# Performance work log

Measured on AMD Instinct MI355X. Metric: run time of the kernel, lower is better.

Reference implementation:

```python
import jax, jax.numpy as jnp
import numpy as np

NA, NH, E, EL, D = 100000, 20000, 1000000, 200000, 128


def _sage(x_src, x_dst, src, dst, W_l, b_l, W_r, num_dst):
    # PyG SAGEConv: out = lin_l(mean_j x_src[j]) + lin_r(x_dst); lin_l has bias, lin_r does not.
    msg = x_src[src]                                   # [E, D] gather
    agg = jax.ops.segment_sum(msg, dst, num_segments=num_dst)   # [num_dst, D]
    deg = jax.ops.segment_sum(jnp.ones((src.shape[0],), x_src.dtype), dst, num_segments=num_dst)
    agg = agg / jnp.maximum(deg, 1.0)[:, None]         # mean aggregation; isolated nodes -> 0
    return agg @ W_l + b_l + x_dst @ W_r


def setup_inputs() -> dict:
    key = jax.random.key(0)
    ks = jax.random.split(key, 24)
    s = 1.0 / np.sqrt(D)
    inp = {
        "x_author": jax.random.normal(ks[0], (NA, D), jnp.float32),
        "x_hotel": jax.random.normal(ks[1], (NH, D), jnp.float32),
        "ei_ah_src": jax.random.randint(ks[2], (E,), 0, NA, jnp.int32),
        "ei_ah_dst": jax.random.randint(ks[3], (E,), 0, NH, jnp.int32),
        "ei_ha_src": jax.random.randint(ks[4], (E,), 0, NH, jnp.int32),
        "ei_ha_dst": jax.random.randint(ks[5], (E,), 0, NA, jnp.int32),
        "eli_row": jax.random.randint(ks[6], (EL,), 0, NA, jnp.int32),
        "eli_col": jax.random.randint(ks[7], (EL,), 0, NH, jnp.int32),
    }
    # per-layer, per-edge-type SAGE weights
    names = ["W1_ah_l", "W1_ah_r", "W1_ha_l", "W1_ha_r", "W2_ah_l", "W2_ah_r", "W2_ha_l", "W2_ha_r"]
    for i, n in enumerate(names):
        inp[n] = jax.random.normal(ks[8 + i], (D, D), jnp.float32) * s
    inp["b1_ah_l"] = jnp.zeros((D,), jnp.float32)
    inp["b1_ha_l"] = jnp.zeros((D,), jnp.float32)
    inp["b2_ah_l"] = jnp.zeros((D,), jnp.float32)
    inp["b2_ha_l"] = jnp.zeros((D,), jnp.float32)
    # decoder MLP
    inp["W_lin1"] = jax.random.normal(ks[16], (2 * D, D), jnp.float32) * (1.0 / np.sqrt(2 * D))
    inp["b_lin1"] = jnp.zeros((D,), jnp.float32)
    inp["W_lin2"] = jax.random.normal(ks[17], (D, 1), jnp.float32) * s
    inp["b_lin2"] = jnp.zeros((1,), jnp.float32)
    return inp


def reference(x_author, x_hotel, ei_ah_src, ei_ah_dst, ei_ha_src, ei_ha_dst,
              eli_row, eli_col,
              W1_ah_l, b1_ah_l, W1_ah_r, W1_ha_l, b1_ha_l, W1_ha_r,
              W2_ah_l, b2_ah_l, W2_ah_r, W2_ha_l, b2_ha_l, W2_ha_r,
              W_lin1, b_lin1, W_lin2, b_lin2):
    # layer 1 (HeteroConv: each node type receives from exactly one edge type) + relu
    h_hotel = jax.nn.relu(_sage(x_author, x_hotel, ei_ah_src, ei_ah_dst, W1_ah_l, b1_ah_l, W1_ah_r, NH))
    h_author = jax.nn.relu(_sage(x_hotel, x_author, ei_ha_src, ei_ha_dst, W1_ha_l, b1_ha_l, W1_ha_r, NA))
    # layer 2 (no relu on last layer)
    z_hotel = _sage(h_author, h_hotel, ei_ah_src, ei_ah_dst, W2_ah_l, b2_ah_l, W2_ah_r, NH)
    z_author = _sage(h_hotel, h_author, ei_ha_src, ei_ha_dst, W2_ha_l, b2_ha_l, W2_ha_r, NA)
    # edge decoder: gather-concat -> 2-layer MLP
    z1 = jnp.concatenate([z_author[eli_row], z_hotel[eli_col]], axis=-1)  # [EL, 2D]
    z2 = jax.nn.relu(z1 @ W_lin1 + b_lin1)                                # [EL, D]
    pred = (z2 @ W_lin2 + b_lin2).reshape(-1)                             # [EL]
    return (pred, z1, z2)
```

## Files before the change

### kernel.cpp

```cpp
#include <hip/hip_runtime.h>

#define NA_ 100000
#define NH_ 20000
#define E_  1000000
#define EL_ 200000
#define D_  128

#define NBH_ 20
#define NBA_ 98
#define NBT_ 118

typedef __attribute__((ext_vector_type(8))) short short8;
typedef __attribute__((ext_vector_type(4))) float f32x4;

__device__ __forceinline__ ushort f2bf(float f) {
  union { float f; uint u; } v; v.f = f;
  uint u = v.u;
  return (ushort)((u + 0x7FFFu + ((u >> 16) & 1u)) >> 16);
}
__device__ __forceinline__ uint pack2bf(float a, float b) {
  return (uint)f2bf(a) | ((uint)f2bf(b) << 16);
}


__global__ __launch_bounds__(256) void cvt_count_k(const float* __restrict__ xa, ushort* __restrict__ da,
                                                   const float* __restrict__ xh, ushort* __restrict__ dh,
                                                   const int* __restrict__ d1, int* __restrict__ c1,
                                                   const int* __restrict__ d2, int* __restrict__ c2) {
  int i = blockIdx.x * 256 + threadIdx.x;
  if (i < E_) atomicAdd(&c1[d1[i]], 1);
  else if (i < 2 * E_) atomicAdd(&c2[d2[i - E_]], 1);
  const int na4 = NA_ * 32;
  if (i < na4) {
    float4 v = *(const float4*)(xa + (size_t)i * 4);
    ((uint2*)da)[i] = make_uint2(pack2bf(v.x, v.y), pack2bf(v.z, v.w));
  } else {
    int k = i - na4;
    if (k < NH_ * 32) {
      float4 v = *(const float4*)(xh + (size_t)k * 4);
      ((uint2*)dh)[k] = make_uint2(pack2bf(v.x, v.y), pack2bf(v.z, v.w));
    }
  }
}


__global__ __launch_bounds__(256) void csr_partial_k(const int* __restrict__ cnt_h,
                                                     const int* __restrict__ cnt_a,
                                                     int* __restrict__ partials) {
  int b = blockIdx.x;
  bool isH = b < NBH_;
  const int* c = isH ? cnt_h : cnt_a;
  int n = isH ? NH_ : NA_;
  int chunk = isH ? b : b - NBH_;
  int t = threadIdx.x;
  int i0 = chunk * 1024 + t * 4;
  int s = 0;
  if (i0 + 3 < n) {
    int4 v = *(const int4*)(c + i0);
    s = v.x + v.y + v.z + v.w;
  } else {
    for (int k = 0; k < 4; k++) if (i0 + k < n) s += c[i0 + k];
  }
#pragma unroll
  for (int d = 1; d < 64; d <<= 1) s += __shfl_xor(s, d);
  __shared__ int ws[4];
  int lane = t & 63, wv = t >> 6;
  if (lane == 0) ws[wv] = s;
  __syncthreads();
  if (t == 0) partials[b] = ws[0] + ws[1] + ws[2] + ws[3];
}


__global__ __launch_bounds__(128) void csr_scanp_k(int* __restrict__ partials,
                                                   int* __restrict__ off_h,
                                                   int* __restrict__ off_a) {
  __shared__ int s[128];
  int t = threadIdx.x;
  int orig = (t < NBT_) ? partials[t] : 0;
  int seg = (t < NBH_) ? 0 : 1;
  s[t] = orig;
  __syncthreads();
  for (int d = 1; d < 128; d <<= 1) {
    int v = 0;
    if (t >= d) {
      int o = t - d;
      if (((o < NBH_) ? 0 : 1) == seg) v = s[o];
    }
    __syncthreads();
    s[t] += v;
    __syncthreads();
  }
  if (t < NBT_) partials[t] = s[t] - orig;
  if (t == 0) { off_h[NH_] = E_; off_a[NA_] = E_; }
}


__global__ __launch_bounds__(256) void csr_scatter_k(int* __restrict__ cnt_h, int* __restrict__ off_h,
                                                     int* __restrict__ cnt_a, int* __restrict__ off_a,
                                                     const int* __restrict__ partials) {
  int b = blockIdx.x;
  bool isH = b < NBH_;
  int* c = isH ? cnt_h : cnt_a;
  int* off = isH ? off_h : off_a;
  int n = isH ? NH_ : NA_;
  int chunk = isH ? b : b - NBH_;
  int t = threadIdx.x, lane = t & 63, wv = t >> 6;
  int base = partials[b];
  int i0 = chunk * 1024 + t * 4;
  int v0 = 0, v1 = 0, v2 = 0, v3 = 0;
  if (i0 + 3 < n) {
    int4 v = *(const int4*)(c + i0);
    v0 = v.x; v1 = v.y; v2 = v.z; v3 = v.w;
  } else {
    if (i0 < n) v0 = c[i0];
    if (i0 + 1 < n) v1 = c[i0 + 1];
    if (i0 + 2 < n) v2 = c[i0 + 2];
    if (i0 + 3 < n) v3 = c[i0 + 3];
  }
  int tsum = v0 + v1 + v2 + v3;
  int x = tsum;
#pragma unroll
  for (int d = 1; d < 64; d <<= 1) { int y = __shfl_up(x, d); if (lane >= d) x += y; }
  __shared__ int ws[4], wb[4];
  if (lane == 63) ws[wv] = x;
  __syncthreads();
  if (t == 0) { int r = 0; for (int i = 0; i < 4; i++) { wb[i] = r; r += ws[i]; } }
  __syncthreads();
  int run = base + wb[wv] + (x - tsum);
  int o0 = run, o1 = o0 + v0, o2 = o1 + v1, o3 = o2 + v2;
  if (i0 + 3 < n) {
    *(int4*)(off + i0) = make_int4(o0, o1, o2, o3);
    *(int4*)(c + i0) = make_int4(o0, o1, o2, o3);
  } else {
    if (i0 < n) { off[i0] = o0; c[i0] = o0; }
    if (i0 + 1 < n) { off[i0 + 1] = o1; c[i0 + 1] = o1; }
    if (i0 + 2 < n) { off[i0 + 2] = o2; c[i0 + 2] = o2; }
    if (i0 + 3 < n) { off[i0 + 3] = o3; c[i0 + 3] = o3; }
  }
}

__global__ void fill_edges_k(const int* __restrict__ s1, const int* __restrict__ d1,
                             int* __restrict__ cur1, int* __restrict__ out1,
                             const int* __restrict__ s2, const int* __restrict__ d2,
                             int* __restrict__ cur2, int* __restrict__ out2) {
  int i = blockIdx.x * 256 + threadIdx.x;
  if (i < E_) {
    int p = atomicAdd(&cur1[d1[i]], 1);
    out1[p] = s1[i];
  } else if (i < 2 * E_) {
    int ii = i - E_;
    int p = atomicAdd(&cur2[d2[ii]], 1);
    out2[p] = s2[ii];
  }
}


__global__ void pack_all_k(const float* a0, const float* a1, ushort* ad,
                           const float* b0, const float* b1, ushort* bd,
                           const float* c0, const float* c1, ushort* cd,
                           const float* d0, const float* d1, ushort* dd,
                           const float* e0, const float* e1, ushort* ed) {
  const float *s0, *s1; ushort* dst;
  switch (blockIdx.y) {
    case 0: s0 = a0; s1 = a1; dst = ad; break;
    case 1: s0 = b0; s1 = b1; dst = bd; break;
    case 2: s0 = c0; s1 = c1; dst = cd; break;
    case 3: s0 = d0; s1 = d1; dst = dd; break;
    default: s0 = e0; s1 = e1; dst = ed; break;
  }
  int idx = blockIdx.x * 256 + threadIdx.x;
  int j = idx & 7, lane = (idx >> 3) & 63, nt = (idx >> 9) & 7, kc = idx >> 12;
  int k = kc * 32 + (lane >> 4) * 8 + j;
  int n = nt * 16 + (lane & 15);
  float v = (k < 128) ? s0[k * 128 + n] : s1[(k - 128) * 128 + n];
  dst[idx] = f2bf(v);
}


__global__ __launch_bounds__(256) void aggregate_bf_k(const ushort* __restrict__ xsrc,
                                                      const int* __restrict__ off,
                                                      const int* __restrict__ srcs,
                                                      ushort* __restrict__ out, int ndst) {
  int w = (blockIdx.x * 256 + threadIdx.x) >> 6;
  int lane = threadIdx.x & 63;
  if (w >= ndst) return;
  const int grp = lane >> 4, sub = lane & 15;
  int beg = off[w], end = off[w + 1];
  float a[8] = {0.f, 0.f, 0.f, 0.f, 0.f, 0.f, 0.f, 0.f};
  const ushort* base = xsrc + sub * 8;
  int j = beg + grp;
  for (; j + 4 < end; j += 8) {
    int sA = srcs[j];
    int sB = srcs[j + 4];
    uint4 vA = *(const uint4*)(base + (size_t)sA * 128);
    uint4 vB = *(const uint4*)(base + (size_t)sB * 128);
    a[0] += __uint_as_float(vA.x << 16); a[1] += __uint_as_float(vA.x & 0xFFFF0000u);
    a[2] += __uint_as_float(vA.y << 16); a[3] += __uint_as_float(vA.y & 0xFFFF0000u);
    a[4] += __uint_as_float(vA.z << 16); a[5] += __uint_as_float(vA.z & 0xFFFF0000u);
    a[6] += __uint_as_float(vA.w << 16); a[7] += __uint_as_float(vA.w & 0xFFFF0000u);
    a[0] += __uint_as_float(vB.x << 16); a[1] += __uint_as_float(vB.x & 0xFFFF0000u);
    a[2] += __uint_as_float(vB.y << 16); a[3] += __uint_as_float(vB.y & 0xFFFF0000u);
    a[4] += __uint_as_float(vB.z << 16); a[5] += __uint_as_float(vB.z & 0xFFFF0000u);
    a[6] += __uint_as_float(vB.w << 16); a[7] += __uint_as_float(vB.w & 0xFFFF0000u);
  }
  if (j < end) {
    int sA = srcs[j];
    uint4 vA = *(const uint4*)(base + (size_t)sA * 128);
    a[0] += __uint_as_float(vA.x << 16); a[1] += __uint_as_float(vA.x & 0xFFFF0000u);
    a[2] += __uint_as_float(vA.y << 16); a[3] += __uint_as_float(vA.y & 0xFFFF0000u);
    a[4] += __uint_as_float(vA.z << 16); a[5] += __uint_as_float(vA.z & 0xFFFF0000u);
    a[6] += __uint_as_float(vA.w << 16); a[7] += __uint_as_float(vA.w & 0xFFFF0000u);
  }
#pragma unroll
  for (int k = 0; k < 8; k++) {
    a[k] += __shfl_xor(a[k], 16);
    a[k] += __shfl_xor(a[k], 32);
  }
  int deg = end - beg;
  float sc = 1.0f / (float)(deg > 0 ? deg : 1);
  if (grp == 0) {
    uint4 o;
    o.x = pack2bf(a[0] * sc, a[1] * sc);
    o.y = pack2bf(a[2] * sc, a[3] * sc);
    o.z = pack2bf(a[4] * sc, a[5] * sc);
    o.w = pack2bf(a[6] * sc, a[7] * sc);
    *(uint4*)(out + (size_t)w * 128 + sub * 8) = o;
  }
}


template <bool RELU, bool OUTBF>
__global__ __launch_bounds__(256) void sage_mfma_k(const ushort* __restrict__ Abf,
                                                   const ushort* __restrict__ Xbf,
                                                   const ushort* __restrict__ Wp,
                                                   const float* __restrict__ bias,
                                                   float* __restrict__ outF,
                                                   ushort* __restrict__ outB, int rows) {
  const int t = threadIdx.x;
  const int w = t >> 6, lane = t & 63, quad = lane >> 4, m = lane & 15;
  const int row0 = blockIdx.x * 64 + w * 16;
  int rA = row0 + m; if (rA >= rows) rA = rows - 1;
  f32x4 acc[8];
#pragma unroll
  for (int nt = 0; nt < 8; nt++) acc[nt] = (f32x4){0.f, 0.f, 0.f, 0.f};
#pragma unroll
  for (int kc = 0; kc < 8; kc++) {
    const ushort* src = (kc < 4) ? (Abf + (size_t)rA * 128 + kc * 32)
                                 : (Xbf + (size_t)rA * 128 + (kc - 4) * 32);
    short8 a = *(const short8*)(src + quad * 8);
    const ushort* wp = Wp + (size_t)(kc * 8) * 512 + lane * 8;
#pragma unroll
    for (int nt = 0; nt < 8; nt++) {
      short8 b = *(const short8*)(wp + nt * 512);
      acc[nt] = __builtin_amdgcn_mfma_f32_16x16x32_bf16(a, b, acc[nt], 0, 0, 0);
    }
  }
#pragma unroll
  for (int nt = 0; nt < 8; nt++) {
    float bv = bias[nt * 16 + m];
#pragma unroll
    for (int r = 0; r < 4; r++) {
      int row = row0 + quad * 4 + r;
      if (row < rows) {
        float v = acc[nt][r] + bv;
        if (RELU) v = fmaxf(v, 0.f);
        if (OUTBF) outB[(size_t)row * 128 + nt * 16 + m] = f2bf(v);
        else       outF[(size_t)row * 128 + nt * 16 + m] = v;
      }
    }
  }
}


__global__ __launch_bounds__(256) void decoder_mfma_k(const float* __restrict__ Za,
                                                      const float* __restrict__ Zh,
                                                      const int* __restrict__ rowi,
                                                      const int* __restrict__ coli,
                                                      const ushort* __restrict__ Wp,
                                                      const float* __restrict__ b1,
                                                      const float* __restrict__ W2,
                                                      const float* __restrict__ b2,
                                                      float* __restrict__ pred,
                                                      float* __restrict__ z1o,
                                                      float* __restrict__ z2o) {
  __shared__ ushort z1bf[64 * 264];
  __shared__ int ra[64], rc[64];
  const int t = threadIdx.x, w = t >> 6, lane = t & 63, quad = lane >> 4, m = lane & 15;
  const int rb = blockIdx.x * 64;
  if (t < 64) ra[t] = rowi[rb + t];
  else if (t < 128) rc[t - 64] = coli[rb + t - 64];
  __syncthreads();
#pragma unroll 4
  for (int rr = 0; rr < 16; rr++) {
    int row = w * 16 + rr;
    int a = ra[row], c = rc[row];
    float2 va = *(const float2*)(Za + (size_t)a * 128 + lane * 2);
    float2 vc = *(const float2*)(Zh + (size_t)c * 128 + lane * 2);
    float* zr = z1o + (size_t)(rb + row) * 256;
    __builtin_nontemporal_store(*(const double*)&va, (double*)(zr + lane * 2));
    __builtin_nontemporal_store(*(const double*)&vc, (double*)(zr + 128 + lane * 2));
    uint* lbase = (uint*)(z1bf + row * 264);
    lbase[lane] = pack2bf(va.x, va.y);
    lbase[64 + lane] = pack2bf(vc.x, vc.y);
  }
  __syncthreads();
  f32x4 acc[8];
#pragma unroll
  for (int nt = 0; nt < 8; nt++) acc[nt] = (f32x4){0.f, 0.f, 0.f, 0.f};
#pragma unroll
  for (int kc = 0; kc < 8; kc++) {
    short8 a = *(const short8*)(z1bf + (w * 16 + m) * 264 + kc * 32 + quad * 8);
    const ushort* wp = Wp + (size_t)(kc * 8) * 512 + lane * 8;
#pragma unroll
    for (int nt = 0; nt < 8; nt++) {
      short8 b = *(const short8*)(wp + nt * 512);
      acc[nt] = __builtin_amdgcn_mfma_f32_16x16x32_bf16(a, b, acc[nt], 0, 0, 0);
    }
  }
  float part[4] = {0.f, 0.f, 0.f, 0.f};
#pragma unroll
  for (int nt = 0; nt < 8; nt++) {
    float bv = b1[nt * 16 + m];
    float wv = W2[nt * 16 + m];
#pragma unroll
    for (int r = 0; r < 4; r++) {
      float v = fmaxf(acc[nt][r] + bv, 0.f);
      __builtin_nontemporal_store(v, z2o + (size_t)(rb + w * 16 + quad * 4 + r) * 128 + nt * 16 + m);
      part[r] += v * wv;
    }
  }
  const float bias2 = b2[0];
#pragma unroll
  for (int r = 0; r < 4; r++) {
    float s = part[r];
    s += __shfl_xor(s, 1); s += __shfl_xor(s, 2);
    s += __shfl_xor(s, 4); s += __shfl_xor(s, 8);
    if (m == 0) pred[rb + w * 16 + quad * 4 + r] = s + bias2;
  }
}


static inline char* carve(char*& p, size_t bytes) {
  char* r = p;
  p += (bytes + 255) & ~(size_t)255;
  return r;
}

extern "C" void kernel_launch(void* const* d_in, const int* in_sizes, int n_in,
                              void* d_out, int out_size, void* d_ws, size_t ws_size,
                              hipStream_t stream) {
  const float* x_author = (const float*)d_in[0];
  const float* x_hotel  = (const float*)d_in[1];
  const int* ei_ah_src  = (const int*)d_in[2];
  const int* ei_ah_dst  = (const int*)d_in[3];
  const int* ei_ha_src  = (const int*)d_in[4];
  const int* ei_ha_dst  = (const int*)d_in[5];
  const int* eli_row    = (const int*)d_in[6];
  const int* eli_col    = (const int*)d_in[7];
  const float* W1_ah_l  = (const float*)d_in[8];
  const float* W1_ah_r  = (const float*)d_in[9];
  const float* W1_ha_l  = (const float*)d_in[10];
  const float* W1_ha_r  = (const float*)d_in[11];
  const float* W2_ah_l  = (const float*)d_in[12];
  const float* W2_ah_r  = (const float*)d_in[13];
  const float* W2_ha_l  = (const float*)d_in[14];
  const float* W2_ha_r  = (const float*)d_in[15];
  const float* b1_ah_l  = (const float*)d_in[16];
  const float* b1_ha_l  = (const float*)d_in[17];
  const float* b2_ah_l  = (const float*)d_in[18];
  const float* b2_ha_l  = (const float*)d_in[19];
  const float* W_lin1   = (const float*)d_in[20];
  const float* b_lin1   = (const float*)d_in[21];
  const float* W_lin2   = (const float*)d_in[22];
  const float* b_lin2   = (const float*)d_in[23];

  char* p = (char*)d_ws;
  ushort* xa_bf = (ushort*)carve(p, (size_t)NA_ * D_ * 2);
  ushort* xh_bf = (ushort*)carve(p, (size_t)NH_ * D_ * 2);
  ushort* A_hbf = (ushort*)carve(p, (size_t)NH_ * D_ * 2);
  ushort* A_abf = (ushort*)carve(p, (size_t)NA_ * D_ * 2);
  ushort* H_hbf = (ushort*)carve(p, (size_t)NH_ * D_ * 2);
  ushort* H_abf = (ushort*)carve(p, (size_t)NA_ * D_ * 2);
  float*  Z_h   = (float*)carve(p, (size_t)NH_ * D_ * 4);
  float*  Z_a   = (float*)carve(p, (size_t)NA_ * D_ * 4);
  ushort* Wp1ah = (ushort*)carve(p, 32768 * 2);
  ushort* Wp1ha = (ushort*)carve(p, 32768 * 2);
  ushort* Wp2ah = (ushort*)carve(p, 32768 * 2);
  ushort* Wp2ha = (ushort*)carve(p, 32768 * 2);
  ushort* WpD   = (ushort*)carve(p, 32768 * 2);
  int* off_h = (int*)carve(p, (size_t)(NH_ + 1) * 4);
  int* off_a = (int*)carve(p, (size_t)(NA_ + 1) * 4);
  int* cur_h = (int*)carve(p, (size_t)(NH_ + NA_) * 4);
  int* cur_a = cur_h + NH_;
  int* s_ah  = (int*)carve(p, (size_t)E_ * 4);
  int* s_ha  = (int*)carve(p, (size_t)E_ * 4);
  int* partials = (int*)carve(p, 256 * 4);

  float* pred = (float*)d_out;
  float* z1o  = pred + EL_;
  float* z2o  = z1o + (size_t)EL_ * 256;

  hipMemsetAsync(cur_h, 0, (size_t)(NH_ + NA_) * 4, stream);
  cvt_count_k<<<(NA_ * 32 + NH_ * 32 + 255) / 256, 256, 0, stream>>>(
      x_author, xa_bf, x_hotel, xh_bf, ei_ah_dst, cur_h, ei_ha_dst, cur_a);

  csr_partial_k<<<NBT_, 256, 0, stream>>>(cur_h, cur_a, partials);
  csr_scanp_k<<<1, 128, 0, stream>>>(partials, off_h, off_a);
  csr_scatter_k<<<NBT_, 256, 0, stream>>>(cur_h, off_h, cur_a, off_a, partials);

  fill_edges_k<<<(2 * E_ + 255) / 256, 256, 0, stream>>>(ei_ah_src, ei_ah_dst, cur_h, s_ah,
                                                         ei_ha_src, ei_ha_dst, cur_a, s_ha);

  dim3 pg(128, 5);
  pack_all_k<<<pg, 256, 0, stream>>>(W1_ah_l, W1_ah_r, Wp1ah,
                                     W1_ha_l, W1_ha_r, Wp1ha,
                                     W2_ah_l, W2_ah_r, Wp2ah,
                                     W2_ha_l, W2_ha_r, Wp2ha,
                                     W_lin1, W_lin1 + 128 * 128, WpD);

  aggregate_bf_k<<<(NH_ + 3) / 4, 256, 0, stream>>>(xa_bf, off_h, s_ah, A_hbf, NH_);
  sage_mfma_k<true, true><<<(NH_ + 63) / 64, 256, 0, stream>>>(A_hbf, xh_bf, Wp1ah, b1_ah_l, nullptr, H_hbf, NH_);
  aggregate_bf_k<<<(NA_ + 3) / 4, 256, 0, stream>>>(xh_bf, off_a, s_ha, A_abf, NA_);
  sage_mfma_k<true, true><<<(NA_ + 63) / 64, 256, 0, stream>>>(A_abf, xa_bf, Wp1ha, b1_ha_l, nullptr, H_abf, NA_);

  aggregate_bf_k<<<(NH_ + 3) / 4, 256, 0, stream>>>(H_abf, off_h, s_ah, A_hbf, NH_);
  sage_mfma_k<false, false><<<(NH_ + 63) / 64, 256, 0, stream>>>(A_hbf, H_hbf, Wp2ah, b2_ah_l, Z_h, nullptr, NH_);
  aggregate_bf_k<<<(NA_ + 3) / 4, 256, 0, stream>>>(H_hbf, off_a, s_ha, A_abf, NA_);
  sage_mfma_k<false, false><<<(NA_ + 63) / 64, 256, 0, stream>>>(A_abf, H_abf, Wp2ha, b2_ha_l, Z_a, nullptr, NA_);

  decoder_mfma_k<<<EL_ / 64, 256, 0, stream>>>(Z_a, Z_h, eli_row, eli_col,
                                               WpD, b_lin1, W_lin2, b_lin2,
                                               pred, z1o, z2o);
}
```

Before: 904.9 us.

## Fuse neighbor mean aggregation into SAGE MFMA kernel and merge both edge types

Replaces separate aggregate and MFMA kernels with one fused kernel per layer that gathers and averages neighbor rows into shared memory, then runs the bf16 MFMA GEMM directly from LDS. Both node types (hotel and author) are handled in a single launch by splitting blocks by index. This removes the round trip of the aggregated bf16 intermediate through global memory and cuts the launch count from eight to two. In exchange, each wave now aggregates 16 rows serially before any MFMA work, which may reduce the parallelism available to hide gather latency.

```diff
diff --git a/kernel.cpp b/kernel.cpp
--- a/kernel.cpp
+++ b/kernel.cpp
@@ -9,6 +9,9 @@
 #define NBH_ 20
 #define NBA_ 98
 #define NBT_ 118
+
+#define FBH_ 313
+#define FBA_ 1563
 
 typedef __attribute__((ext_vector_type(8))) short short8;
 typedef __attribute__((ext_vector_type(4))) float f32x4;
@@ -70,7 +73,6 @@
   if (t == 0) partials[b] = ws[0] + ws[1] + ws[2] + ws[3];
 }
 
-
 __global__ __launch_bounds__(128) void csr_scanp_k(int* __restrict__ partials,
                                                    int* __restrict__ off_h,
                                                    int* __restrict__ off_a) {
@@ -93,7 +95,6 @@
   if (t < NBT_) partials[t] = s[t] - orig;
   if (t == 0) { off_h[NH_] = E_; off_a[NA_] = E_; }
 }
-
 
 __global__ __launch_bounds__(256) void csr_scatter_k(int* __restrict__ cnt_h, int* __restrict__ off_h,
                                                      int* __restrict__ cnt_a, int* __restrict__ off_a,
@@ -177,82 +178,98 @@
 }
 
 
-__global__ __launch_bounds__(256) void aggregate_bf_k(const ushort* __restrict__ xsrc,
-                                                      const int* __restrict__ off,
-                                                      const int* __restrict__ srcs,
-                                                      ushort* __restrict__ out, int ndst) {
-  int w = (blockIdx.x * 256 + threadIdx.x) >> 6;
-  int lane = threadIdx.x & 63;
-  if (w >= ndst) return;
+template <bool RELU, bool OUTBF>
+__global__ __launch_bounds__(256) void sage_fused_k(
+    const int* __restrict__ off0, const int* __restrict__ src0,
+    const ushort* __restrict__ G0, const ushort* __restrict__ X0,
+    const ushort* __restrict__ W0, const float* __restrict__ B0,
+    ushort* __restrict__ oB0, float* __restrict__ oF0, int n0, int nb0,
+    const int* __restrict__ off1, const int* __restrict__ src1,
+    const ushort* __restrict__ G1, const ushort* __restrict__ X1,
+    const ushort* __restrict__ W1, const float* __restrict__ B1,
+    ushort* __restrict__ oB1, float* __restrict__ oF1, int n1) {
+  const int b = blockIdx.x;
+  const bool p0 = b < nb0;
+  const int* off = p0 ? off0 : off1;
+  const int* srcs = p0 ? src0 : src1;
+  const ushort* G = p0 ? G0 : G1;
+  const ushort* X = p0 ? X0 : X1;
+  const ushort* Wp = p0 ? W0 : W1;
+  const float* bias = p0 ? B0 : B1;
+  ushort* outB = p0 ? oB0 : oB1;
+  float* outF = p0 ? oF0 : oF1;
+  const int rows = p0 ? n0 : n1;
+  const int rb = (p0 ? b : b - nb0) * 64;
+
+  __shared__ ushort At[64 * 136];
+
+  const int t = threadIdx.x, w = t >> 6, lane = t & 63;
   const int grp = lane >> 4, sub = lane & 15;
-  int beg = off[w], end = off[w + 1];
-  float a[8] = {0.f, 0.f, 0.f, 0.f, 0.f, 0.f, 0.f, 0.f};
-  const ushort* base = xsrc + sub * 8;
-  int j = beg + grp;
-  for (; j + 4 < end; j += 8) {
-    int sA = srcs[j];
-    int sB = srcs[j + 4];
-    uint4 vA = *(const uint4*)(base + (size_t)sA * 128);
-    uint4 vB = *(const uint4*)(base + (size_t)sB * 128);
-    a[0] += __uint_as_float(vA.x << 16); a[1] += __uint_as_float(vA.x & 0xFFFF0000u);
-    a[2] += __uint_as_float(vA.y << 16); a[3] += __uint_as_float(vA.y & 0xFFFF0000u);
-    a[4] += __uint_as_float(vA.z << 16); a[5] += __uint_as_float(vA.z & 0xFFFF0000u);
-    a[6] += __uint_as_float(vA.w << 16); a[7] += __uint_as_float(vA.w & 0xFFFF0000u);
-    a[0] += __uint_as_float(vB.x << 16); a[1] += __uint_as_float(vB.x & 0xFFFF0000u);
-    a[2] += __uint_as_float(vB.y << 16); a[3] += __uint_as_float(vB.y & 0xFFFF0000u);
-    a[4] += __uint_as_float(vB.z << 16); a[5] += __uint_as_float(vB.z & 0xFFFF0000u);
-    a[6] += __uint_as_float(vB.w << 16); a[7] += __uint_as_float(vB.w & 0xFFFF0000u);
-  }
-  if (j < end) {
-    int sA = srcs[j];
-    uint4 vA = *(const uint4*)(base + (size_t)sA * 128);
-    a[0] += __uint_as_float(vA.x << 16); a[1] += __uint_as_float(vA.x & 0xFFFF0000u);
-    a[2] += __uint_as_float(vA.y << 16); a[3] += __uint_as_float(vA.y & 0xFFFF0000u);
-    a[4] += __uint_as_float(vA.z << 16); a[5] += __uint_as_float(vA.z & 0xFFFF0000u);
-    a[6] += __uint_as_float(vA.w << 16); a[7] += __uint_as_float(vA.w & 0xFFFF0000u);
-  }
-#pragma unroll
-  for (int k = 0; k < 8; k++) {
-    a[k] += __shfl_xor(a[k], 16);
-    a[k] += __shfl_xor(a[k], 32);
-  }
-  int deg = end - beg;
-  float sc = 1.0f / (float)(deg > 0 ? deg : 1);
-  if (grp == 0) {
-    uint4 o;
-    o.x = pack2bf(a[0] * sc, a[1] * sc);
-    o.y = pack2bf(a[2] * sc, a[3] * sc);
-    o.z = pack2bf(a[4] * sc, a[5] * sc);
-    o.w = pack2bf(a[6] * sc, a[7] * sc);
-    *(uint4*)(out + (size_t)w * 128 + sub * 8) = o;
-  }
-}
-
-
-template <bool RELU, bool OUTBF>
-__global__ __launch_bounds__(256) void sage_mfma_k(const ushort* __restrict__ Abf,
-                                                   const ushort* __restrict__ Xbf,
-                                                   const ushort* __restrict__ Wp,
-                                                   const float* __restrict__ bias,
-                                                   float* __restrict__ outF,
-                                                   ushort* __restrict__ outB, int rows) {
-  const int t = threadIdx.x;
-  const int w = t >> 6, lane = t & 63, quad = lane >> 4, m = lane & 15;
-  const int row0 = blockIdx.x * 64 + w * 16;
-  int rA = row0 + m; if (rA >= rows) rA = rows - 1;
+  const ushort* gbase = G + sub * 8;
+
+  for (int rr = 0; rr < 16; rr++) {
+    int row = rb + w * 16 + rr;
+    float a[8] = {0.f, 0.f, 0.f, 0.f, 0.f, 0.f, 0.f, 0.f};
+    int deg = 0;
+    if (row < rows) {
+      int beg = off[row], end = off[row + 1];
+      deg = end - beg;
+      int j = beg + grp;
+      for (; j + 4 < end; j += 8) {
+        int sA = srcs[j];
+        int sB = srcs[j + 4];
+        uint4 vA = *(const uint4*)(gbase + (size_t)sA * 128);
+        uint4 vB = *(const uint4*)(gbase + (size_t)sB * 128);
+        a[0] += __uint_as_float(vA.x << 16); a[1] += __uint_as_float(vA.x & 0xFFFF0000u);
+        a[2] += __uint_as_float(vA.y << 16); a[3] += __uint_as_float(vA.y & 0xFFFF0000u);
+        a[4] += __uint_as_float(vA.z << 16); a[5] += __uint_as_float(vA.z & 0xFFFF0000u);
+        a[6] += __uint_as_float(vA.w << 16); a[7] += __uint_as_float(vA.w & 0xFFFF0000u);
+        a[0] += __uint_as_float(vB.x << 16); a[1] += __uint_as_float(vB.x & 0xFFFF0000u);
+        a[2] += __uint_as_float(vB.y << 16); a[3] += __uint_as_float(vB.y & 0xFFFF0000u);
+        a[4] += __uint_as_float(vB.z << 16); a[5] += __uint_as_float(vB.z & 0xFFFF0000u);
+        a[6] += __uint_as_float(vB.w << 16); a[7] += __uint_as_float(vB.w & 0xFFFF0000u);
+      }
+      if (j < end) {
+        int sA = srcs[j];
+        uint4 vA = *(const uint4*)(gbase + (size_t)sA * 128);
+        a[0] += __uint_as_float(vA.x << 16); a[1] += __uint_as_float(vA.x & 0xFFFF0000u);
+        a[2] += __uint_as_float(vA.y << 16); a[3] += __uint_as_float(vA.y & 0xFFFF0000u);
+        a[4] += __uint_as_float(vA.z << 16); a[5] += __uint_as_float(vA.z & 0xFFFF0000u);
+        a[6] += __uint_as_float(vA.w << 16); a[7] += __uint_as_float(vA.w & 0xFFFF0000u);
+      }
+#pragma unroll
+      for (int k = 0; k < 8; k++) {
+        a[k] += __shfl_xor(a[k], 16);
+        a[k] += __shfl_xor(a[k], 32);
+      }
+    }
+    if (grp == 0) {
+      float sc = 1.0f / (float)(deg > 0 ? deg : 1);
+      uint4 o;
+      o.x = pack2bf(a[0] * sc, a[1] * sc);
+      o.y = pack2bf(a[2] * sc, a[3] * sc);
+      o.z = pack2bf(a[4] * sc, a[5] * sc);
+      o.w = pack2bf(a[6] * sc, a[7] * sc);
+      *(uint4*)(At + (w * 16 + rr) * 136 + sub * 8) = o;
+    }
+  }
+  __syncthreads();
+
+  const int quad = lane >> 4, m = lane & 15;
+  int rA = rb + w * 16 + m; if (rA >= rows) rA = rows - 1;
   f32x4 acc[8];
 #pragma unroll
   for (int nt = 0; nt < 8; nt++) acc[nt] = (f32x4){0.f, 0.f, 0.f, 0.f};
 #pragma unroll
   for (int kc = 0; kc < 8; kc++) {
-    const ushort* src = (kc < 4) ? (Abf + (size_t)rA * 128 + kc * 32)
-                                 : (Xbf + (size_t)rA * 128 + (kc - 4) * 32);
-    short8 a = *(const short8*)(src + quad * 8);
+    short8 a;
+    if (kc < 4) a = *(const short8*)(At + (w * 16 + m) * 136 + kc * 32 + quad * 8);
+    else        a = *(const short8*)(X + (size_t)rA * 128 + (kc - 4) * 32 + quad * 8);
     const ushort* wp = Wp + (size_t)(kc * 8) * 512 + lane * 8;
 #pragma unroll
     for (int nt = 0; nt < 8; nt++) {
-      short8 b = *(const short8*)(wp + nt * 512);
-      acc[nt] = __builtin_amdgcn_mfma_f32_16x16x32_bf16(a, b, acc[nt], 0, 0, 0);
+      short8 bfr = *(const short8*)(wp + nt * 512);
+      acc[nt] = __builtin_amdgcn_mfma_f32_16x16x32_bf16(a, bfr, acc[nt], 0, 0, 0);
     }
   }
 #pragma unroll
@@ -260,7 +277,7 @@
     float bv = bias[nt * 16 + m];
 #pragma unroll
     for (int r = 0; r < 4; r++) {
-      int row = row0 + quad * 4 + r;
+      int row = rb + w * 16 + quad * 4 + r;
       if (row < rows) {
         float v = acc[nt][r] + bv;
         if (RELU) v = fmaxf(v, 0.f);
@@ -377,8 +394,6 @@
   char* p = (char*)d_ws;
   ushort* xa_bf = (ushort*)carve(p, (size_t)NA_ * D_ * 2);
   ushort* xh_bf = (ushort*)carve(p, (size_t)NH_ * D_ * 2);
-  ushort* A_hbf = (ushort*)carve(p, (size_t)NH_ * D_ * 2);
-  ushort* A_abf = (ushort*)carve(p, (size_t)NA_ * D_ * 2);
   ushort* H_hbf = (ushort*)carve(p, (size_t)NH_ * D_ * 2);
   ushort* H_abf = (ushort*)carve(p, (size_t)NA_ * D_ * 2);
   float*  Z_h   = (float*)carve(p, (size_t)NH_ * D_ * 4);
@@ -418,15 +433,13 @@
                                      W2_ha_l, W2_ha_r, Wp2ha,
                                      W_lin1, W_lin1 + 128 * 128, WpD);
 
-  aggregate_bf_k<<<(NH_ + 3) / 4, 256, 0, stream>>>(xa_bf, off_h, s_ah, A_hbf, NH_);
-  sage_mfma_k<true, true><<<(NH_ + 63) / 64, 256, 0, stream>>>(A_hbf, xh_bf, Wp1ah, b1_ah_l, nullptr, H_hbf, NH_);
-  aggregate_bf_k<<<(NA_ + 3) / 4, 256, 0, stream>>>(xh_bf, off_a, s_ha, A_abf, NA_);
-  sage_mfma_k<true, true><<<(NA_ + 63) / 64, 256, 0, stream>>>(A_abf, xa_bf, Wp1ha, b1_ha_l, nullptr, H_abf, NA_);
-
-  aggregate_bf_k<<<(NH_ + 3) / 4, 256, 0, stream>>>(H_abf, off_h, s_ah, A_hbf, NH_);
-  sage_mfma_k<false, false><<<(NH_ + 63) / 64, 256, 0, stream>>>(A_hbf, H_hbf, Wp2ah, b2_ah_l, Z_h, nullptr, NH_);
-  aggregate_bf_k<<<(NA_ + 3) / 4, 256, 0, stream>>>(H_hbf, off_a, s_ha, A_abf, NA_);
-  sage_mfma_k<false, false><<<(NA_ + 63) / 64, 256, 0, stream>>>(A_abf, H_abf, Wp2ha, b2_ha_l, Z_a, nullptr, NA_);
+  sage_fused_k<true, true><<<FBH_ + FBA_, 256, 0, stream>>>(
+      off_h, s_ah, xa_bf, xh_bf, Wp1ah, b1_ah_l, H_hbf, nullptr, NH_, FBH_,
+      off_a, s_ha, xh_bf, xa_bf, Wp1ha, b1_ha_l, H_abf, nullptr, NA_);
+
+  sage_fused_k<false, false><<<FBH_ + FBA_, 256, 0, stream>>>(
+      off_h, s_ah, H_abf, H_hbf, Wp2ah, b2_ah_l, nullptr, Z_h, NH_, FBH_,
+      off_a, s_ha, H_hbf, H_abf, Wp2ha, b2_ha_l, nullptr, Z_a, NA_);
 
   decoder_mfma_k<<<EL_ / 64, 256, 0, stream>>>(Z_a, Z_h, eli_row, eli_col,
                                                WpD, b_lin1, W_lin2, b_lin2,
```

Result: no change. 890.1 us (-1.6%).
